# Performance work log

Hardware: AMD Instinct MI355X
Metric: run time of the kernel (lower is better)

The kernel has to match this reference:

```python
import jax, jax.numpy as jnp
import numpy as np

B, CV, CP, X, Y, Z = 4, 16, 16, 256, 256, 32
NV, NORIG, NSLOT, D = 100000, 131072, 50, 256
CC = CV + CP  # combined_feature_dim = 32


def _l2norm(x, axis):
    n = jnp.linalg.norm(x, axis=axis, keepdims=True)
    return x / jnp.maximum(n, 1e-12)


def _group_norm(x, gamma, beta, groups=4, eps=1e-5):
    # x: [B, C, L]; normalize over (C//groups, L) per group, like nn.GroupNorm
    b, c, l = x.shape
    xg = x.reshape(b, groups, c // groups, l)
    mu = xg.mean(axis=(2, 3), keepdims=True)
    var = xg.var(axis=(2, 3), keepdims=True)
    xg = (xg - mu) / jnp.sqrt(var + eps)
    return xg.reshape(b, c, l) * gamma[None, :, None] + beta[None, :, None]


def setup_inputs() -> dict:
    key = jax.random.key(0)
    ks = jax.random.split(key, 10)
    voxel_feats_dense = jax.random.normal(ks[0], (B, CV, X, Y, Z), dtype=jnp.float32)
    raw_point_feats = jax.random.normal(ks[1], (B, NV, CP), dtype=jnp.float32)
    slot = jax.random.normal(ks[2], (B, NSLOT, D), dtype=jnp.float32)
    # voxel_coords columns: [:,0] indexes Z, [:,1] indexes Y, [:,2] indexes X
    c0 = jax.random.randint(ks[3], (B, NV), 0, Z)
    c1 = jax.random.randint(ks[4], (B, NV), 0, Y)
    c2 = jax.random.randint(ks[5], (B, NV), 0, X)
    voxel_coords = jnp.stack([c0, c1, c2], axis=-1).astype(jnp.int32)
    # unique scatter targets per batch (voxelizer keeps a subset of raw points)
    point_idxes = jnp.stack([
        jax.random.permutation(jax.random.fold_in(ks[6], i), NORIG)[:NV]
        for i in range(B)
    ]).astype(jnp.int32)
    W1 = jax.random.normal(ks[7], (D, D), dtype=jnp.float32) * 0.05
    b1 = jnp.zeros((D,), jnp.float32)
    gn_gamma = jnp.ones((D,), jnp.float32)
    gn_beta = jnp.zeros((D,), jnp.float32)
    W2 = jax.random.normal(ks[8], (CC, D), dtype=jnp.float32) * 0.05
    b2 = jnp.zeros((CC,), jnp.float32)
    return dict(voxel_feats_dense=voxel_feats_dense, raw_point_feats=raw_point_feats,
                slot=slot, W1=W1, b1=b1, gn_gamma=gn_gamma, gn_beta=gn_beta,
                W2=W2, b2=b2, voxel_coords=voxel_coords, point_idxes=point_idxes,
                n_original=NORIG)


def reference(voxel_feats_dense, raw_point_feats, slot, W1, b1, gn_gamma, gn_beta,
              W2, b2, voxel_coords, point_idxes, n_original):
    b, cv, xd, yd, zd = voxel_feats_dense.shape
    vc = voxel_coords
    # voxel-to-point gather: dense[i, :, vc[:,2], vc[:,1], vc[:,0]].T
    lin = vc[..., 2] * (yd * zd) + vc[..., 1] * zd + vc[..., 0]  # [B, NV]
    flat = voxel_feats_dense.reshape(b, cv, -1)
    interp = jnp.take_along_axis(flat, lin[:, None, :], axis=2)  # [B, CV, NV]
    padded_feats = jnp.concatenate([jnp.transpose(interp, (0, 2, 1)),
                                    raw_point_feats], axis=-1)   # [B, NV, CC]
    # object_mlp on slot.transpose(1,2): conv1d(k=1) -> GroupNorm(4) -> ReLU -> conv1d(k=1)
    st = jnp.transpose(slot, (0, 2, 1))                           # [B, D, NSLOT]
    h = jnp.einsum('oc,bcn->bon', W1, st) + b1[None, :, None]
    h = jax.nn.relu(_group_norm(h, gn_gamma, gn_beta))
    slot_proj = jnp.einsum('oc,bcn->bon', W2, h) + b2[None, :, None]  # [B, CC, NSLOT]
    # cosine similarity mask with temperature 0.05
    mask = jnp.einsum('bnc,bck->bnk', _l2norm(padded_feats, 2),
                      _l2norm(slot_proj, 1)) / 0.05                # [B, NV, NSLOT]
    k = mask.shape[2]
    # scatter back to original point indices (zeros elsewhere)
    scatter = jax.vmap(lambda m, idx: jnp.zeros((n_original, k), m.dtype).at[idx].set(m))(
        mask, point_idxes)                                         # [B, NORIG, NSLOT]
    final = jnp.transpose(scatter.reshape(b * n_original, k), (1, 0))  # [NSLOT, B*NORIG]
    return jax.nn.softmax(final, axis=0)
```

## Files before the change

kernel.cpp:

```cpp
#include <hip/hip_runtime.h>

#define BB     4
#define CVC    16
#define CPC    16
#define CCC    32
#define XD     256
#define YD     256
#define ZD     32
#define NVX    100000
#define NORIG  131072
#define NSLOT  50
#define DD     256
#define XYZ    (XD*YD*ZD)
#define BN     ((size_t)BB*NORIG)

__global__ __launch_bounds__(256) void fill_kernel(int* __restrict__ inv,
                                                   float* __restrict__ stats){
  int i = blockIdx.x*256 + threadIdx.x;
  if (i < (int)BN) inv[i] = -1;
  if (i < 32) stats[i] = 0.f;
}

__global__ __launch_bounds__(256) void scatter_kernel(const int* __restrict__ pidx,
                                                      int* __restrict__ inv){
  int t = blockIdx.x*256 + threadIdx.x;
  if (t < BB*NVX){
    int b = t / NVX;
    int n = t - b*NVX;
    inv[b*NORIG + pidx[t]] = n;
  }
}

__global__ __launch_bounds__(256) void mlp1_kernel(
    const float* __restrict__ slot, const float* __restrict__ W1,
    const float* __restrict__ b1, float* __restrict__ ws_h,
    float* __restrict__ stats){
  int s = blockIdx.x, b = blockIdx.y, d = threadIdx.x;
  __shared__ float sv[DD];
  sv[d] = slot[((size_t)b*NSLOT + s)*DD + d];
  __syncthreads();
  const float4* w1q = (const float4*)(W1 + (size_t)d*DD);
  float acc = b1[d];
  #pragma unroll
  for (int q = 0; q < 64; q++){
    float4 w = w1q[q];
    const float* sp = &sv[q*4];
    acc = fmaf(w.x, sp[0], acc);
    acc = fmaf(w.y, sp[1], acc);
    acc = fmaf(w.z, sp[2], acc);
    acc = fmaf(w.w, sp[3], acc);
  }
  ws_h[((size_t)b*NSLOT + s)*DD + d] = acc;
  float s1 = acc, s2 = acc*acc;
  #pragma unroll
  for (int off = 32; off > 0; off >>= 1){
    s1 += __shfl_down(s1, off, 64);
    s2 += __shfl_down(s2, off, 64);
  }
  if ((d & 63) == 0){
    int g = d >> 6;
    atomicAdd(&stats[(b*4+g)*2+0], s1);
    atomicAdd(&stats[(b*4+g)*2+1], s2);
  }
}

__global__ __launch_bounds__(256) void mlp2_kernel(
    const float* __restrict__ ws_h, const float* __restrict__ stats,
    const float* __restrict__ gamma, const float* __restrict__ beta,
    const float* __restrict__ W2, const float* __restrict__ b2,
    float* __restrict__ slotn){
  int s = blockIdx.x, b = blockIdx.y, d = threadIdx.x;
  float h = ws_h[((size_t)b*NSLOT + s)*DD + d];
  int g = d >> 6;
  float s1 = stats[(b*4+g)*2+0];
  float s2 = stats[(b*4+g)*2+1];
  const float invN = 1.f/3200.f;
  float mean = s1*invN;
  float var  = s2*invN - mean*mean;
  float hn = (h - mean) * rsqrtf(var + 1e-5f) * gamma[d] + beta[d];
  hn = fmaxf(hn, 0.f);
  __shared__ float hsh[DD];
  __shared__ float red[256];
  __shared__ float spo[CCC];
  hsh[d] = hn;
  __syncthreads();
  int o = d & 31, ch = d >> 5;
  const float4* w2q = (const float4*)(W2 + (size_t)o*DD + ch*32);
  float p = 0.f;
  #pragma unroll
  for (int q = 0; q < 8; q++){
    float4 w = w2q[q];
    const float* hp = &hsh[ch*32 + q*4];
    p = fmaf(w.x, hp[0], p);
    p = fmaf(w.y, hp[1], p);
    p = fmaf(w.z, hp[2], p);
    p = fmaf(w.w, hp[3], p);
  }
  red[d] = p;
  __syncthreads();
  if (ch == 0){
    float sp = b2[o];
    #pragma unroll
    for (int c = 0; c < 8; c++) sp += red[c*32 + o];
    spo[o] = sp;
  }
  __syncthreads();
  if (d < CCC){
    float ss = 0.f;
    #pragma unroll
    for (int o2 = 0; o2 < CCC; o2++) ss += spo[o2]*spo[o2];
    float sc = 20.f / fmaxf(sqrtf(ss), 1e-12f);
    slotn[((size_t)b*NSLOT + s)*CCC + d] = spo[d]*sc;
  }
}

__global__ __launch_bounds__(256, 6) void main_kernel(
    const float* __restrict__ vox, const float* __restrict__ raw,
    const int* __restrict__ coords, const int* __restrict__ inv,
    const float* __restrict__ slotn, float* __restrict__ out){
  __shared__ float ssl[NSLOT*CCC];
  int b = blockIdx.y;
  {
    const float4* src = (const float4*)(slotn + (size_t)b*NSLOT*CCC);
    float4* dst = (float4*)ssl;
    #pragma unroll
    for (int i = threadIdx.x; i < (NSLOT*CCC)/4; i += 256) dst[i] = src[i];
  }
  __syncthreads();
  int col = blockIdx.x*256 + threadIdx.x;
  int n = inv[b*NORIG + col];
  float* op = out + (size_t)b*NORIG + col;
  if (n >= 0){
    const int* vc = coords + 3*((size_t)b*NVX + n);
    int c0 = vc[0], c1 = vc[1], c2 = vc[2];
    int lin = c2*(YD*ZD) + c1*ZD + c0;
    const float* vb = vox + (size_t)b*CVC*XYZ + lin;
    float f[CCC];
    const float4* rp = (const float4*)(raw + (size_t)CPC*((size_t)b*NVX + n));
    float4 q0 = rp[0], q1 = rp[1], q2 = rp[2], q3 = rp[3];
    #pragma unroll
    for (int c = 0; c < CVC; c++) f[c] = vb[(size_t)c*XYZ];
    f[16] = q0.x; f[17] = q0.y; f[18] = q0.z; f[19] = q0.w;
    f[20] = q1.x; f[21] = q1.y; f[22] = q1.z; f[23] = q1.w;
    f[24] = q2.x; f[25] = q2.y; f[26] = q2.z; f[27] = q2.w;
    f[28] = q3.x; f[29] = q3.y; f[30] = q3.z; f[31] = q3.w;
    float ss = 0.f;
    #pragma unroll
    for (int i = 0; i < CCC; i++) ss = fmaf(f[i], f[i], ss);
    float invn = 1.f / fmaxf(sqrtf(ss), 1e-12f);
    #pragma unroll
    for (int i = 0; i < CCC; i++) f[i] *= invn;
    float sum = 0.f;
    #pragma unroll 2
    for (int k = 0; k < NSLOT; k++){
      const float4* sp = (const float4*)(ssl + k*CCC);
      float acc = 0.f;
      #pragma unroll
      for (int q = 0; q < 8; q++){
        float4 v = sp[q];
        acc = fmaf(f[q*4+0], v.x, acc);
        acc = fmaf(f[q*4+1], v.y, acc);
        acc = fmaf(f[q*4+2], v.z, acc);
        acc = fmaf(f[q*4+3], v.w, acc);
      }
      sum += __expf(acc);
    }
    float rs = 1.f / sum;
    #pragma unroll 2
    for (int k = 0; k < NSLOT; k++){
      const float4* sp = (const float4*)(ssl + k*CCC);
      float acc = 0.f;
      #pragma unroll
      for (int q = 0; q < 8; q++){
        float4 v = sp[q];
        acc = fmaf(f[q*4+0], v.x, acc);
        acc = fmaf(f[q*4+1], v.y, acc);
        acc = fmaf(f[q*4+2], v.z, acc);
        acc = fmaf(f[q*4+3], v.w, acc);
      }
      op[(size_t)k*BN] = __expf(acc) * rs;
    }
  } else {
    #pragma unroll
    for (int k = 0; k < NSLOT; k++) op[(size_t)k*BN] = 0.02f;
  }
}

extern "C" void kernel_launch(void* const* d_in, const int* in_sizes, int n_in,
                              void* d_out, int out_size, void* d_ws, size_t ws_size,
                              hipStream_t stream) {
  (void)in_sizes; (void)n_in; (void)out_size; (void)ws_size;
  const float* vox    = (const float*)d_in[0];
  const float* raw    = (const float*)d_in[1];
  const float* slot   = (const float*)d_in[2];
  const float* W1     = (const float*)d_in[3];
  const float* b1     = (const float*)d_in[4];
  const float* gamma  = (const float*)d_in[5];
  const float* beta   = (const float*)d_in[6];
  const float* W2     = (const float*)d_in[7];
  const float* b2     = (const float*)d_in[8];
  const int*   coords = (const int*)d_in[9];
  const int*   pidx   = (const int*)d_in[10];
  float*       out    = (float*)d_out;

  int*   inv   = (int*)d_ws;
  float* stats = (float*)((char*)d_ws + BN*sizeof(int));
  float* slotn = stats + 32;
  float* ws_h  = slotn + (size_t)BB*NSLOT*CCC;

  fill_kernel   <<<dim3((unsigned)((BN + 255)/256)), 256, 0, stream>>>(inv, stats);
  scatter_kernel<<<dim3((BB*NVX + 255)/256),          256, 0, stream>>>(pidx, inv);
  mlp1_kernel   <<<dim3(NSLOT, BB),                   256, 0, stream>>>(slot, W1, b1, ws_h, stats);
  mlp2_kernel   <<<dim3(NSLOT, BB),                   256, 0, stream>>>(ws_h, stats, gamma, beta, W2, b2, slotn);
  main_kernel   <<<dim3(NORIG/256, BB),               256, 0, stream>>>(vox, raw, coords, inv, slotn, out);
}
```

Baseline: 834.3 us.

## Precompute voxel linear index in scatter and read slot vectors from global

The scatter kernel now computes each point's linear voxel index from its coords and stores it next to the point index as an int2. The main kernel therefore skips the dependent coords gather before the voxel gather. The main kernel also stops staging the normalized slot vectors in shared memory and reads them directly from global memory with fully unrolled loops, which drops the block-wide sync. In exchange, the index buffer write and read traffic doubles, and uniform global loads plus heavier unrolling may raise register pressure.

```diff
diff --git a/kernel.cpp b/kernel.cpp
--- a/kernel.cpp
+++ b/kernel.cpp
@@ -14,20 +14,23 @@
 #define XYZ    (XD*YD*ZD)
 #define BN     ((size_t)BB*NORIG)
 
-__global__ __launch_bounds__(256) void fill_kernel(int* __restrict__ inv,
+__global__ __launch_bounds__(256) void fill_kernel(int2* __restrict__ il,
                                                    float* __restrict__ stats){
   int i = blockIdx.x*256 + threadIdx.x;
-  if (i < (int)BN) inv[i] = -1;
+  if (i < (int)BN) il[i] = make_int2(-1, 0);
   if (i < 32) stats[i] = 0.f;
 }
 
 __global__ __launch_bounds__(256) void scatter_kernel(const int* __restrict__ pidx,
-                                                      int* __restrict__ inv){
+                                                      const int* __restrict__ coords,
+                                                      int2* __restrict__ il){
   int t = blockIdx.x*256 + threadIdx.x;
   if (t < BB*NVX){
     int b = t / NVX;
     int n = t - b*NVX;
-    inv[b*NORIG + pidx[t]] = n;
+    const int* vc = coords + 3*(size_t)t;
+    int lin = vc[2]*(YD*ZD) + vc[1]*ZD + vc[0];
+    il[(size_t)b*NORIG + pidx[t]] = make_int2(n, lin);
   }
 }
 
@@ -116,30 +119,20 @@
 
 __global__ __launch_bounds__(256, 6) void main_kernel(
     const float* __restrict__ vox, const float* __restrict__ raw,
-    const int* __restrict__ coords, const int* __restrict__ inv,
-    const float* __restrict__ slotn, float* __restrict__ out){
-  __shared__ float ssl[NSLOT*CCC];
+    const int2* __restrict__ il, const float* __restrict__ slotn,
+    float* __restrict__ out){
   int b = blockIdx.y;
-  {
-    const float4* src = (const float4*)(slotn + (size_t)b*NSLOT*CCC);
-    float4* dst = (float4*)ssl;
-    #pragma unroll
-    for (int i = threadIdx.x; i < (NSLOT*CCC)/4; i += 256) dst[i] = src[i];
-  }
-  __syncthreads();
   int col = blockIdx.x*256 + threadIdx.x;
-  int n = inv[b*NORIG + col];
+  int2 t = il[(size_t)b*NORIG + col];
   float* op = out + (size_t)b*NORIG + col;
+  int n = t.x;
   if (n >= 0){
-    const int* vc = coords + 3*((size_t)b*NVX + n);
-    int c0 = vc[0], c1 = vc[1], c2 = vc[2];
-    int lin = c2*(YD*ZD) + c1*ZD + c0;
-    const float* vb = vox + (size_t)b*CVC*XYZ + lin;
+    const float* vb = vox + (size_t)b*CVC*XYZ + (size_t)t.y;
     float f[CCC];
+    #pragma unroll
+    for (int c = 0; c < CVC; c++) f[c] = vb[(size_t)c*XYZ];
     const float4* rp = (const float4*)(raw + (size_t)CPC*((size_t)b*NVX + n));
     float4 q0 = rp[0], q1 = rp[1], q2 = rp[2], q3 = rp[3];
-    #pragma unroll
-    for (int c = 0; c < CVC; c++) f[c] = vb[(size_t)c*XYZ];
     f[16] = q0.x; f[17] = q0.y; f[18] = q0.z; f[19] = q0.w;
     f[20] = q1.x; f[21] = q1.y; f[22] = q1.z; f[23] = q1.w;
     f[24] = q2.x; f[25] = q2.y; f[26] = q2.z; f[27] = q2.w;
@@ -150,10 +143,11 @@
     float invn = 1.f / fmaxf(sqrtf(ss), 1e-12f);
     #pragma unroll
     for (int i = 0; i < CCC; i++) f[i] *= invn;
+    const float* sb = slotn + (size_t)b*NSLOT*CCC;
     float sum = 0.f;
-    #pragma unroll 2
+    #pragma unroll
     for (int k = 0; k < NSLOT; k++){
-      const float4* sp = (const float4*)(ssl + k*CCC);
+      const float4* sp = (const float4*)(sb + k*CCC);
       float acc = 0.f;
       #pragma unroll
       for (int q = 0; q < 8; q++){
@@ -166,9 +160,9 @@
       sum += __expf(acc);
     }
     float rs = 1.f / sum;
-    #pragma unroll 2
+    #pragma unroll
     for (int k = 0; k < NSLOT; k++){
-      const float4* sp = (const float4*)(ssl + k*CCC);
+      const float4* sp = (const float4*)(sb + k*CCC);
       float acc = 0.f;
       #pragma unroll
       for (int q = 0; q < 8; q++){
@@ -203,14 +197,14 @@
   const int*   pidx   = (const int*)d_in[10];
   float*       out    = (float*)d_out;
 
-  int*   inv   = (int*)d_ws;
-  float* stats = (float*)((char*)d_ws + BN*sizeof(int));
+  int2*  il    = (int2*)d_ws;
+  float* stats = (float*)((char*)d_ws + BN*sizeof(int2));
   float* slotn = stats + 32;
   float* ws_h  = slotn + (size_t)BB*NSLOT*CCC;
 
-  fill_kernel   <<<dim3((unsigned)((BN + 255)/256)), 256, 0, stream>>>(inv, stats);
-  scatter_kernel<<<dim3((BB*NVX + 255)/256),          256, 0, stream>>>(pidx, inv);
+  fill_kernel   <<<dim3((unsigned)((BN + 255)/256)), 256, 0, stream>>>(il, stats);
+  scatter_kernel<<<dim3((BB*NVX + 255)/256),          256, 0, stream>>>(pidx, coords, il);
   mlp1_kernel   <<<dim3(NSLOT, BB),                   256, 0, stream>>>(slot, W1, b1, ws_h, stats);
   mlp2_kernel   <<<dim3(NSLOT, BB),                   256, 0, stream>>>(ws_h, stats, gamma, beta, W2, b2, slotn);
-  main_kernel   <<<dim3(NORIG/256, BB),               256, 0, stream>>>(vox, raw, coords, inv, slotn, out);
-}
+  main_kernel   <<<dim3(NORIG/256, BB),               256, 0, stream>>>(vox, raw, il, slotn, out);
+}
```

Result: slower. 959.3 us (+15.0%).
